# Kernel optimization log

Measured on AMD Instinct MI355X. Metric: run time of the kernel, lower is better.

Reference implementation:

```python
import jax, jax.numpy as jnp
import numpy as np

N, P, K, LF = 1024, 20000, 8, 1  # samples, in_features(=fold_num at stride 1), kernel_size, local_feature


def setup_inputs() -> dict:
    key = jax.random.key(0)
    k1, k2 = jax.random.split(key)
    X = jax.random.normal(k1, (N, P), dtype=jnp.float32)
    # GlorotUniform over weight tensor (fold_num, kernel_size, local_feature)
    limit = np.sqrt(6.0 / (K + LF)).astype(np.float32)
    W = jax.random.uniform(k2, (P, K, LF), dtype=jnp.float32, minval=-limit, maxval=limit)
    b = jnp.zeros((P, LF), dtype=jnp.float32)
    return {"X": X, "W": W, "b": b}


def reference(X, W, b):
    # Pad right by kernel_size-1 (same as tf.pad with [[0,0],[0,K-1]])
    Xp = jnp.pad(X, ((0, 0), (0, K - 1)))  # [N, P+K-1]
    # im2col: sliding windows of length K at stride 1 -> [N, P, K]
    idx = jnp.arange(P)[:, None] + jnp.arange(K)[None, :]  # [P, K]
    patches = Xp[:, idx]  # [N, P, K]
    # per-position matmul with distinct weights W[p] in R^{KxLF}, LF=1
    AL = jnp.einsum('npk,pkl->npl', patches, W) + b  # [N, P, 1]
    return AL.reshape(X.shape[0], P)  # [N, P]
```

## Files before the change

### kernel.cpp

```cpp
#include <hip/hip_runtime.h>


constexpr int N  = 1024;
constexpr int P  = 20000;
constexpr int K  = 8;
constexpr int P4 = P / 4;
constexpr int COLS_PADDED = 5120;
constexpr int NCHUNKS = 64;
constexpr int ROWS = N / NCHUNKS;

__global__ __launch_bounds__(256)
void local_linear_kernel(const float* __restrict__ X,
                         const float* __restrict__ W,
                         const float* __restrict__ b,
                         float* __restrict__ out) {
    int tid   = blockIdx.x * blockDim.x + threadIdx.x;
    int chunk = tid / COLS_PADDED;
    int q     = tid - chunk * COLS_PADDED;
    if (q >= P4) return;

    int p  = q * 4;
    int n0 = chunk * ROWS;

    const float* wp = W + (size_t)p * K;
    float wv[32];
    #pragma unroll
    for (int i = 0; i < 8; ++i) {
        float4 w4 = *reinterpret_cast<const float4*>(wp + i * 4);
        wv[i * 4 + 0] = w4.x;
        wv[i * 4 + 1] = w4.y;
        wv[i * 4 + 2] = w4.z;
        wv[i * 4 + 3] = w4.w;
    }
    float4 bv = *reinterpret_cast<const float4*>(b + p);

    const bool interior = (p + 12 <= P);

    for (int r = 0; r < ROWS; ++r) {
        const float* xrow = X + (size_t)(n0 + r) * P;

        float xv[12];
        if (interior) {
            float4 a = *reinterpret_cast<const float4*>(xrow + p);
            float4 c = *reinterpret_cast<const float4*>(xrow + p + 4);
            float4 d = *reinterpret_cast<const float4*>(xrow + p + 8);
            xv[0] = a.x; xv[1] = a.y; xv[2]  = a.z; xv[3]  = a.w;
            xv[4] = c.x; xv[5] = c.y; xv[6]  = c.z; xv[7]  = c.w;
            xv[8] = d.x; xv[9] = d.y; xv[10] = d.z; xv[11] = d.w;
        } else {
            #pragma unroll
            for (int i = 0; i < 12; ++i)
                xv[i] = (p + i < P) ? xrow[p + i] : 0.0f;
        }

        float r0 = bv.x, r1 = bv.y, r2 = bv.z, r3 = bv.w;
        #pragma unroll
        for (int k = 0; k < K; ++k) {
            r0 += xv[0 + k] * wv[0  + k];
            r1 += xv[1 + k] * wv[8  + k];
            r2 += xv[2 + k] * wv[16 + k];
            r3 += xv[3 + k] * wv[24 + k];
        }

        float4 o; o.x = r0; o.y = r1; o.z = r2; o.w = r3;
        *reinterpret_cast<float4*>(out + (size_t)(n0 + r) * P + p) = o;
    }
}

extern "C" void kernel_launch(void* const* d_in, const int* in_sizes, int n_in,
                              void* d_out, int out_size, void* d_ws, size_t ws_size,
                              hipStream_t stream) {
    const float* X = (const float*)d_in[0];
    const float* W = (const float*)d_in[1];
    const float* b = (const float*)d_in[2];
    float* out = (float*)d_out;

    constexpr int total_threads = COLS_PADDED * NCHUNKS;
    constexpr int block = 256;
    constexpr int grid = total_threads / block;

    local_linear_kernel<<<grid, block, 0, stream>>>(X, W, b, out);
}
```

Baseline: 35.14 us.

## Stage weights through padded LDS and double the row-chunk count

Each block now loads its weight slice into shared memory with coalesced float4 reads. The LDS layout is padded to avoid bank conflicts, and each thread then reads its 32 weights from LDS instead of doing strided per-thread global float4 loads. NCHUNKS doubles to 128, so each thread handles fewer rows, the grid has more blocks and occupancy rises (launch_bounds 256,4). The row loop is unrolled by 2. The trade-off is that weights are re-read from global memory twice as often in total, and a block-wide sync plus LDS traffic is added.

```diff
diff --git a/kernel.cpp b/kernel.cpp
--- a/kernel.cpp
+++ b/kernel.cpp
@@ -4,38 +4,60 @@
 constexpr int N  = 1024;
 constexpr int P  = 20000;
 constexpr int K  = 8;
+constexpr int PK = P * K;
 constexpr int P4 = P / 4;
 constexpr int COLS_PADDED = 5120;
-constexpr int NCHUNKS = 64;
+constexpr int NCHUNKS = 128;
 constexpr int ROWS = N / NCHUNKS;
 
-__global__ __launch_bounds__(256)
+constexpr int TILE_W_FLOATS = 256 * 32;
+constexpr int LDS_FLOATS = TILE_W_FLOATS + TILE_W_FLOATS/32;
+
+__device__ __forceinline__ int pad_idx(int l) { return l + (l >> 5); }
+
+__global__ __launch_bounds__(256, 4)
 void local_linear_kernel(const float* __restrict__ X,
                          const float* __restrict__ W,
                          const float* __restrict__ b,
                          float* __restrict__ out) {
-    int tid   = blockIdx.x * blockDim.x + threadIdx.x;
-    int chunk = tid / COLS_PADDED;
-    int q     = tid - chunk * COLS_PADDED;
+    __shared__ float wsh[LDS_FLOATS];
+
+    const int t     = threadIdx.x;
+    const int tid   = blockIdx.x * blockDim.x + t;
+    const int chunk = tid / COLS_PADDED;
+    const int q     = tid - chunk * COLS_PADDED;
+    const int q0    = q - t;
+    const int p     = q * 4;
+    const int n0    = chunk * ROWS;
+
+    const int wbase = q0 * 32;
+    #pragma unroll
+    for (int i = 0; i < 8; ++i) {
+        int c    = t + 256 * i;
+        int gidx = wbase + 4 * c;
+        float4 w4 = make_float4(0.f, 0.f, 0.f, 0.f);
+        if (gidx + 3 < PK)
+            w4 = *reinterpret_cast<const float4*>(W + gidx);
+        int l = 4 * c;
+        int ph = pad_idx(l);
+        wsh[ph + 0] = w4.x;
+        wsh[ph + 1] = w4.y;
+        wsh[ph + 2] = w4.z;
+        wsh[ph + 3] = w4.w;
+    }
+    __syncthreads();
+
     if (q >= P4) return;
 
-    int p  = q * 4;
-    int n0 = chunk * ROWS;
-
-    const float* wp = W + (size_t)p * K;
     float wv[32];
     #pragma unroll
-    for (int i = 0; i < 8; ++i) {
-        float4 w4 = *reinterpret_cast<const float4*>(wp + i * 4);
-        wv[i * 4 + 0] = w4.x;
-        wv[i * 4 + 1] = w4.y;
-        wv[i * 4 + 2] = w4.z;
-        wv[i * 4 + 3] = w4.w;
-    }
-    float4 bv = *reinterpret_cast<const float4*>(b + p);
+    for (int j = 0; j < 32; ++j)
+        wv[j] = wsh[33 * t + j];
 
+    const float4 bv = *reinterpret_cast<const float4*>(b + p);
     const bool interior = (p + 12 <= P);
 
+    #pragma unroll 2
     for (int r = 0; r < ROWS; ++r) {
         const float* xrow = X + (size_t)(n0 + r) * P;
 
```

After: 37.17 us. 1.06x slower.

## Transpose weights into workspace and double row chunks for coalesced weight loads

Applied to the files above, without the earlier changes.

Adds a pre-pass kernel that transposes W from [P,K] to [K,P] in the workspace. The main kernel can then load each weight tap as a coalesced float4 across adjacent positions instead of eight strided float4 loads per thread. It also doubles NCHUNKS to spawn more threads with fewer rows each, and adds launch bounds and a 2x row unroll. The cost is an extra kernel launch and the transpose traffic on every call, plus more redundant weight loads because more threads are launched; the old path is kept as a fallback when the workspace is too small.

```diff
diff --git a/kernel.cpp b/kernel.cpp
--- a/kernel.cpp
+++ b/kernel.cpp
@@ -6,36 +6,42 @@
 constexpr int K  = 8;
 constexpr int P4 = P / 4;
 constexpr int COLS_PADDED = 5120;
-constexpr int NCHUNKS = 64;
+constexpr int NCHUNKS = 128;
 constexpr int ROWS = N / NCHUNKS;
 
 __global__ __launch_bounds__(256)
+void transpose_w(const float* __restrict__ W, float* __restrict__ Wt) {
+    int p = blockIdx.x * blockDim.x + threadIdx.x;
+    if (p >= P) return;
+    float4 a = *reinterpret_cast<const float4*>(W + (size_t)p * K);
+    float4 c = *reinterpret_cast<const float4*>(W + (size_t)p * K + 4);
+    Wt[0 * P + p] = a.x; Wt[1 * P + p] = a.y;
+    Wt[2 * P + p] = a.z; Wt[3 * P + p] = a.w;
+    Wt[4 * P + p] = c.x; Wt[5 * P + p] = c.y;
+    Wt[6 * P + p] = c.z; Wt[7 * P + p] = c.w;
+}
+
+__global__ __launch_bounds__(256, 4)
 void local_linear_kernel(const float* __restrict__ X,
-                         const float* __restrict__ W,
+                         const float* __restrict__ Wt,
                          const float* __restrict__ b,
                          float* __restrict__ out) {
-    int tid   = blockIdx.x * blockDim.x + threadIdx.x;
-    int chunk = tid / COLS_PADDED;
-    int q     = tid - chunk * COLS_PADDED;
+    const int tid   = blockIdx.x * blockDim.x + threadIdx.x;
+    const int chunk = tid / COLS_PADDED;
+    const int q     = tid - chunk * COLS_PADDED;
     if (q >= P4) return;
+    const int p  = q * 4;
+    const int n0 = chunk * ROWS;
 
-    int p  = q * 4;
-    int n0 = chunk * ROWS;
-
-    const float* wp = W + (size_t)p * K;
-    float wv[32];
+    float4 wv[8];
     #pragma unroll
-    for (int i = 0; i < 8; ++i) {
-        float4 w4 = *reinterpret_cast<const float4*>(wp + i * 4);
-        wv[i * 4 + 0] = w4.x;
-        wv[i * 4 + 1] = w4.y;
-        wv[i * 4 + 2] = w4.z;
-        wv[i * 4 + 3] = w4.w;
-    }
-    float4 bv = *reinterpret_cast<const float4*>(b + p);
+    for (int k = 0; k < K; ++k)
+        wv[k] = *reinterpret_cast<const float4*>(Wt + (size_t)k * P + p);
+    const float4 bv = *reinterpret_cast<const float4*>(b + p);
 
     const bool interior = (p + 12 <= P);
 
+    #pragma unroll 2
     for (int r = 0; r < ROWS; ++r) {
         const float* xrow = X + (size_t)(n0 + r) * P;
 
@@ -56,12 +62,62 @@
         float r0 = bv.x, r1 = bv.y, r2 = bv.z, r3 = bv.w;
         #pragma unroll
         for (int k = 0; k < K; ++k) {
+            r0 += xv[k + 0] * wv[k].x;
+            r1 += xv[k + 1] * wv[k].y;
+            r2 += xv[k + 2] * wv[k].z;
+            r3 += xv[k + 3] * wv[k].w;
+        }
+
+        float4 o; o.x = r0; o.y = r1; o.z = r2; o.w = r3;
+        *reinterpret_cast<float4*>(out + (size_t)(n0 + r) * P + p) = o;
+    }
+}
+
+__global__ __launch_bounds__(256)
+void local_linear_fallback(const float* __restrict__ X,
+                           const float* __restrict__ W,
+                           const float* __restrict__ b,
+                           float* __restrict__ out) {
+    const int tid   = blockIdx.x * blockDim.x + threadIdx.x;
+    const int chunk = tid / COLS_PADDED;
+    const int q     = tid - chunk * COLS_PADDED;
+    if (q >= P4) return;
+    const int p  = q * 4;
+    const int n0 = chunk * ROWS;
+
+    const float* wp = W + (size_t)p * K;
+    float wv[32];
+    #pragma unroll
+    for (int i = 0; i < 8; ++i) {
+        float4 w4 = *reinterpret_cast<const float4*>(wp + i * 4);
+        wv[i*4+0] = w4.x; wv[i*4+1] = w4.y; wv[i*4+2] = w4.z; wv[i*4+3] = w4.w;
+    }
+    const float4 bv = *reinterpret_cast<const float4*>(b + p);
+    const bool interior = (p + 12 <= P);
+
+    for (int r = 0; r < ROWS; ++r) {
+        const float* xrow = X + (size_t)(n0 + r) * P;
+        float xv[12];
+        if (interior) {
+            float4 a = *reinterpret_cast<const float4*>(xrow + p);
+            float4 c = *reinterpret_cast<const float4*>(xrow + p + 4);
+            float4 d = *reinterpret_cast<const float4*>(xrow + p + 8);
+            xv[0]=a.x; xv[1]=a.y; xv[2]=a.z; xv[3]=a.w;
+            xv[4]=c.x; xv[5]=c.y; xv[6]=c.z; xv[7]=c.w;
+            xv[8]=d.x; xv[9]=d.y; xv[10]=d.z; xv[11]=d.w;
+        } else {
+            #pragma unroll
+            for (int i = 0; i < 12; ++i)
+                xv[i] = (p + i < P) ? xrow[p + i] : 0.0f;
+        }
+        float r0 = bv.x, r1 = bv.y, r2 = bv.z, r3 = bv.w;
+        #pragma unroll
+        for (int k = 0; k < K; ++k) {
             r0 += xv[0 + k] * wv[0  + k];
             r1 += xv[1 + k] * wv[8  + k];
             r2 += xv[2 + k] * wv[16 + k];
             r3 += xv[3 + k] * wv[24 + k];
         }
-
         float4 o; o.x = r0; o.y = r1; o.z = r2; o.w = r3;
         *reinterpret_cast<float4*>(out + (size_t)(n0 + r) * P + p) = o;
     }
@@ -78,6 +134,13 @@
     constexpr int total_threads = COLS_PADDED * NCHUNKS;
     constexpr int block = 256;
     constexpr int grid = total_threads / block;
+    constexpr size_t WT_BYTES = (size_t)P * K * sizeof(float);
 
-    local_linear_kernel<<<grid, block, 0, stream>>>(X, W, b, out);
+    if (ws_size >= WT_BYTES) {
+        float* Wt = (float*)d_ws;
+        transpose_w<<<(P + block - 1) / block, block, 0, stream>>>(W, Wt);
+        local_linear_kernel<<<grid, block, 0, stream>>>(X, Wt, b, out);
+    } else {
+        local_linear_fallback<<<grid, block, 0, stream>>>(X, W, b, out);
+    }
 }
```

Result: slower. 37.25 us (+6.0%).
